# Performance work log

Hardware: AMD Instinct MI355X
Metric: run time of the kernel (lower is better)

Reference implementation:

```python
import jax, jax.numpy as jnp
import numpy as np

N = 8192
BOX = 50.0
CUTOFF = 5.0
MAX_E = 64 * N  # padded edge capacity (~34 avg neighbors expected)


def setup_inputs() -> dict:
    key = jax.random.key(0)
    pos = jax.random.uniform(key, (N, 3), dtype=jnp.float32) * BOX
    return {"pos": pos}


def _pairwise_dist(pos):
    # Euclidean cdist via the gram-matrix identity; avoids the [N,N,3] intermediate.
    sq = jnp.sum(pos * pos, axis=-1)                      # [N]
    d2 = sq[:, None] + sq[None, :] - 2.0 * (pos @ pos.T)  # [N,N]
    return jnp.sqrt(jnp.maximum(d2, 0.0))


def reference(pos):
    n = pos.shape[0]
    dist = _pairwise_dist(pos)
    # mask self-edges by pushing the diagonal above the cutoff (as in the torch code)
    dist = dist + (CUTOFF + 1.0) * jnp.eye(n, dtype=dist.dtype)
    mask = dist < CUTOFF
    # data-dependent nonzero -> fixed-size padded output for jit compatibility;
    # padded entries are filled with -1.
    rows, cols = jnp.nonzero(mask, size=MAX_E, fill_value=-1)
    return jnp.stack([rows, cols], axis=0)  # [2, MAX_E], int32
```

## Files before the change

### kernel.cpp

```cpp
#include <hip/hip_runtime.h>
#include <stdint.h>

#define N 8192
#define MAX_E (64 * N)
#define NCOL1 9
#define NCELLS (NCOL1 * NCOL1 * NCOL1)
#define CAP 40
#define RCAP 128
#define SCALE (9.0f / 50.0f)
#define POISON 0xAAAAAAAAu
#define M_WAVES 4
#define E_BLOCKS 256
#define E_ROWS 32

__device__ __forceinline__ float sq_exact(float x, float y, float z) {
    return __fadd_rn(__fadd_rn(__fmul_rn(x, x), __fmul_rn(y, y)), __fmul_rn(z, z));
}

__device__ __forceinline__ bool edge_pred(float xi, float yi, float zi, float sqi,
                                          float px, float py, float pz) {
    float sqj = sq_exact(px, py, pz);
    float dot = __fmaf_rn(zi, pz, __fmaf_rn(yi, py, __fmul_rn(xi, px)));
    float d2  = __fmaf_rn(-2.0f, dot, __fadd_rn(sqi, sqj));
    return d2 < 0x1.8ffffep+4f;
}

__device__ __forceinline__ int cell_of(float v) {
    int c = (int)(__fmul_rn(v, SCALE));
    return c > 8 ? 8 : c;
}

__device__ __forceinline__ int cell3_of(float x, float y, float z) {
    return (cell_of(x) * NCOL1 + cell_of(y)) * NCOL1 + cell_of(z);
}

__global__ __launch_bounds__(256) void bin_kernel(const float* __restrict__ posf,
                                                  unsigned* __restrict__ gcount,
                                                  float4* __restrict__ colpts) {
    const int i = blockIdx.x * 256 + threadIdx.x;
    float x = posf[3 * i], y = posf[3 * i + 1], z = posf[3 * i + 2];
    const int cell = cell3_of(x, y, z);
    unsigned p = atomicAdd(&gcount[cell], 1u) - POISON;
    if (p < CAP) {
        colpts[cell * CAP + p] = make_float4(x, y, z, __int_as_float(i));
    }
}

__global__ __launch_bounds__(256) void mask_kernel(const float* __restrict__ posf,
                                                   const unsigned* __restrict__ gcount,
                                                   const float4* __restrict__ colpts,
                                                   uint16_t* __restrict__ stage,
                                                   int* __restrict__ counts,
                                                   int* __restrict__ out) {
    __shared__ uint32_t lmask[M_WAVES][256];
    const int tid  = threadIdx.x;
    const int wave = tid >> 6;
    const int lane = tid & 63;
    const int row  = blockIdx.x * M_WAVES + wave;

    int2 neg; neg.x = -1; neg.y = -1;
    ((int2*)out)[blockIdx.x * 256 + tid] = neg;

#pragma unroll
    for (int k = lane; k < 256; k += 64) lmask[wave][k] = 0;
    __builtin_amdgcn_wave_barrier();

    const float xi = posf[3 * row], yi = posf[3 * row + 1], zi = posf[3 * row + 2];
    const float sqi = sq_exact(xi, yi, zi);
    const int cx = cell_of(xi), cy = cell_of(yi), cz = cell_of(zi);
    const int zlo = (cz > 0) ? cz - 1 : 0;
    const int zhi = (cz < 8) ? cz + 1 : 8;

    for (int dx = -1; dx <= 1; dx++) {
        const int nx = cx + dx;
        if ((unsigned)nx > 8u) continue;
        for (int dy = -1; dy <= 1; dy++) {
            const int ny = cy + dy;
            if ((unsigned)ny > 8u) continue;
            const int c0 = (nx * NCOL1 + ny) * NCOL1 + zlo;
            int l0 = (int)(gcount[c0] - POISON);     l0 = l0 > CAP ? CAP : l0;
            int l1 = (int)(gcount[c0 + 1] - POISON); l1 = l1 > CAP ? CAP : l1;
            int l2 = 0;
            if (zhi - zlo == 2) {
                l2 = (int)(gcount[c0 + 2] - POISON); l2 = l2 > CAP ? CAP : l2;
            }
            const int t01 = l0 + l1;
            const int tot = t01 + l2;
            for (int k = lane; k < tot; k += 64) {
                const int cellk = c0 + (k >= l0) + (k >= t01);
                const int off = k - ((k >= l0) ? l0 : 0) - ((k >= t01) ? l1 : 0);
                float4 pj = colpts[cellk * CAP + off];
                const int j = __float_as_int(pj.w);
                if (j != row && edge_pred(xi, yi, zi, sqi, pj.x, pj.y, pj.z))
                    atomicOr(&lmask[wave][j >> 5], 1u << (j & 31));
            }
        }
    }
    __builtin_amdgcn_wave_barrier();

    uint4 u = ((const uint4*)lmask[wave])[lane];
    uint64_t k0 = (uint64_t)u.x | ((uint64_t)u.y << 32);
    uint64_t k1 = (uint64_t)u.z | ((uint64_t)u.w << 32);
    const int pc = __popcll(k0) + __popcll(k1);
    int xs = pc;
#pragma unroll
    for (int o = 1; o < 64; o <<= 1) {
        int t = __shfl_up(xs, o);
        if (lane >= o) xs += t;
    }
    if (lane == 63) counts[row] = xs;
    int off = xs - pc;

    uint16_t* dst = stage + (size_t)row * RCAP;
    const int col0 = lane * 128;
    uint64_t m = k0;
    while (m) {
        int b = __ffsll((unsigned long long)m) - 1;
        m &= m - 1;
        if (off < RCAP) dst[off] = (uint16_t)(col0 + b);
        off++;
    }
    m = k1;
    while (m) {
        int b = __ffsll((unsigned long long)m) - 1;
        m &= m - 1;
        if (off < RCAP) dst[off] = (uint16_t)(col0 + 64 + b);
        off++;
    }
}

__global__ __launch_bounds__(256) void emit_kernel(const uint16_t* __restrict__ stage,
                                                   const int* __restrict__ counts,
                                                   int* __restrict__ out) {
    const int tid  = threadIdx.x;
    const int wave = tid >> 6;
    const int lane = tid & 63;
    const int row0 = blockIdx.x * E_ROWS;

    __shared__ int incl[256];
    __shared__ int wtot[4];
    __shared__ int excl32[32];

    const int4* c4 = (const int4*)counts;
    int s = 0;
#pragma unroll
    for (int k = 0; k < 8; k++) {
        int4 v = c4[tid * 8 + k];
        s += v.x + v.y + v.z + v.w;
    }
    int x = s;
#pragma unroll
    for (int o = 1; o < 64; o <<= 1) {
        int t = __shfl_up(x, o);
        if (lane >= o) x += t;
    }
    if (lane == 63) wtot[wave] = x;

    if (tid < 32) {
        int c = counts[row0 + tid];
        int y = c;
#pragma unroll
        for (int o = 1; o < 32; o <<= 1) {
            int t = __shfl_up(y, o, 32);
            if (tid >= o) y += t;
        }
        excl32[tid] = y - c;
    }
    __syncthreads();
    int woff = 0;
#pragma unroll
    for (int w = 0; w < 3; w++) woff += (wave > w) ? wtot[w] : 0;
    incl[tid] = woff + x;
    __syncthreads();
    const int base = (blockIdx.x > 0) ? incl[blockIdx.x - 1] : 0;

#pragma unroll
    for (int r = 0; r < 8; r++) {
        const int lr  = wave * 8 + r;
        const int row = row0 + lr;
        int c = counts[row];
        c = c > RCAP ? RCAP : c;
        const int slot = base + excl32[lr];
        const uint16_t* src = stage + (size_t)row * RCAP;
        for (int k = lane; k < c; k += 64) {
            const int sk = slot + k;
            if (sk < MAX_E) {
                out[sk] = row;
                out[MAX_E + sk] = (int)src[k];
            }
        }
    }
}

extern "C" void kernel_launch(void* const* d_in, const int* in_sizes, int n_in,
                              void* d_out, int out_size, void* d_ws, size_t ws_size,
                              hipStream_t stream) {
    const float* posf = (const float*)d_in[0];
    int* out = (int*)d_out;
    char* ws = (char*)d_ws;
    int*      counts = (int*)ws;
    unsigned* gcount = (unsigned*)(ws + (64 << 10));
    float4*   colpts = (float4*)(ws + (256 << 10));
    uint16_t* stage  = (uint16_t*)(ws + (1 << 20));

    bin_kernel<<<N / 256, 256, 0, stream>>>(posf, gcount, colpts);
    mask_kernel<<<N / M_WAVES, 256, 0, stream>>>(posf, gcount, colpts,
                                                 stage, counts, out);
    emit_kernel<<<E_BLOCKS, 256, 0, stream>>>(stage, counts, out);
}
```

Before: 74.52 us.

## Switch to compacted cell list with fine z-bins and contiguous neighbor ranges

Replaces the fixed-capacity 9x9x9 cell bins with a counting-sort cell list over 9x9x32 cells, using a count kernel, a prefix-scan and scatter kernel, and a global cell-base array. Each row in the mask kernel then scans one contiguous range per (x,y) column, covering only the z-cells within the cutoff margin. This cuts candidate pairs in z and removes the per-element cell and offset index math. The cost is an extra kernel launch and a redundant per-block prefix scan. It also relies on the workspace counters being poisoned to a known value.

```diff
diff --git a/kernel.cpp b/kernel.cpp
--- a/kernel.cpp
+++ b/kernel.cpp
@@ -4,10 +4,13 @@
 #define N 8192
 #define MAX_E (64 * N)
 #define NCOL1 9
-#define NCELLS (NCOL1 * NCOL1 * NCOL1)
-#define CAP 40
+#define NZ 32
+#define NCELLSF (NCOL1 * NCOL1 * NZ)
+#define CPT 11
 #define RCAP 128
 #define SCALE (9.0f / 50.0f)
+#define ZSCALE (32.0f / 50.0f)
+#define ZMARGIN 5.01f
 #define POISON 0xAAAAAAAAu
 #define M_WAVES 4
 #define E_BLOCKS 256
@@ -29,25 +32,74 @@
     int c = (int)(__fmul_rn(v, SCALE));
     return c > 8 ? 8 : c;
 }
-
-__device__ __forceinline__ int cell3_of(float x, float y, float z) {
-    return (cell_of(x) * NCOL1 + cell_of(y)) * NCOL1 + cell_of(z);
-}
-
-__global__ __launch_bounds__(256) void bin_kernel(const float* __restrict__ posf,
-                                                  unsigned* __restrict__ gcount,
-                                                  float4* __restrict__ colpts) {
+__device__ __forceinline__ int zcell_of(float v) {
+    int c = (int)(__fmul_rn(v, ZSCALE));
+    c = c < 0 ? 0 : c;
+    return c > (NZ - 1) ? (NZ - 1) : c;
+}
+__device__ __forceinline__ int cellf_of(float x, float y, float z) {
+    return (cell_of(x) * NCOL1 + cell_of(y)) * NZ + zcell_of(z);
+}
+
+__global__ __launch_bounds__(256) void count_kernel(const float* __restrict__ posf,
+                                                    unsigned* __restrict__ gcount) {
     const int i = blockIdx.x * 256 + threadIdx.x;
     float x = posf[3 * i], y = posf[3 * i + 1], z = posf[3 * i + 2];
-    const int cell = cell3_of(x, y, z);
-    unsigned p = atomicAdd(&gcount[cell], 1u) - POISON;
-    if (p < CAP) {
-        colpts[cell * CAP + p] = make_float4(x, y, z, __int_as_float(i));
-    }
+    atomicAdd(&gcount[cellf_of(x, y, z)], 1u);
+}
+
+__global__ __launch_bounds__(256) void scatter_kernel(const float* __restrict__ posf,
+                                                      const unsigned* __restrict__ gcount,
+                                                      unsigned* __restrict__ cursor,
+                                                      int* __restrict__ cbase_g,
+                                                      float4* __restrict__ colpts) {
+    __shared__ int cb[NCELLSF];
+    __shared__ int wtot[4];
+    const int tid  = threadIdx.x;
+    const int wave = tid >> 6;
+    const int lane = tid & 63;
+
+    int cnt[CPT];
+    int s = 0;
+#pragma unroll
+    for (int k = 0; k < CPT; k++) {
+        const int idx = tid * CPT + k;
+        cnt[k] = (idx < NCELLSF) ? (int)(gcount[idx] - POISON) : 0;
+        s += cnt[k];
+    }
+    int x = s;
+#pragma unroll
+    for (int o = 1; o < 64; o <<= 1) {
+        int t = __shfl_up(x, o);
+        if (lane >= o) x += t;
+    }
+    if (lane == 63) wtot[wave] = x;
+    __syncthreads();
+    int woff = 0;
+#pragma unroll
+    for (int w = 0; w < 3; w++) woff += (wave > w) ? wtot[w] : 0;
+    int run = woff + x - s;
+#pragma unroll
+    for (int k = 0; k < CPT; k++) {
+        const int idx = tid * CPT + k;
+        if (idx < NCELLSF) {
+            cb[idx] = run;
+            if (blockIdx.x == 0) cbase_g[idx] = run;
+            run += cnt[k];
+        }
+    }
+    if (blockIdx.x == 0 && tid == 255) cbase_g[NCELLSF] = woff + x;
+    __syncthreads();
+
+    const int i = blockIdx.x * 256 + tid;
+    float px = posf[3 * i], py = posf[3 * i + 1], pz = posf[3 * i + 2];
+    const int cell = cellf_of(px, py, pz);
+    const int slot = cb[cell] + (int)(atomicAdd(&cursor[cell], 1u) - POISON);
+    colpts[slot] = make_float4(px, py, pz, __int_as_float(i));
 }
 
 __global__ __launch_bounds__(256) void mask_kernel(const float* __restrict__ posf,
-                                                   const unsigned* __restrict__ gcount,
+                                                   const int* __restrict__ cbase,
                                                    const float4* __restrict__ colpts,
                                                    uint16_t* __restrict__ stage,
                                                    int* __restrict__ counts,
@@ -67,9 +119,9 @@
 
     const float xi = posf[3 * row], yi = posf[3 * row + 1], zi = posf[3 * row + 2];
     const float sqi = sq_exact(xi, yi, zi);
-    const int cx = cell_of(xi), cy = cell_of(yi), cz = cell_of(zi);
-    const int zlo = (cz > 0) ? cz - 1 : 0;
-    const int zhi = (cz < 8) ? cz + 1 : 8;
+    const int cx = cell_of(xi), cy = cell_of(yi);
+    const int zlo = zcell_of(__fadd_rn(zi, -ZMARGIN));
+    const int zhi = zcell_of(__fadd_rn(zi,  ZMARGIN));
 
     for (int dx = -1; dx <= 1; dx++) {
         const int nx = cx + dx;
@@ -77,19 +129,11 @@
         for (int dy = -1; dy <= 1; dy++) {
             const int ny = cy + dy;
             if ((unsigned)ny > 8u) continue;
-            const int c0 = (nx * NCOL1 + ny) * NCOL1 + zlo;
-            int l0 = (int)(gcount[c0] - POISON);     l0 = l0 > CAP ? CAP : l0;
-            int l1 = (int)(gcount[c0 + 1] - POISON); l1 = l1 > CAP ? CAP : l1;
-            int l2 = 0;
-            if (zhi - zlo == 2) {
-                l2 = (int)(gcount[c0 + 2] - POISON); l2 = l2 > CAP ? CAP : l2;
-            }
-            const int t01 = l0 + l1;
-            const int tot = t01 + l2;
-            for (int k = lane; k < tot; k += 64) {
-                const int cellk = c0 + (k >= l0) + (k >= t01);
-                const int off = k - ((k >= l0) ? l0 : 0) - ((k >= t01) ? l1 : 0);
-                float4 pj = colpts[cellk * CAP + off];
+            const int cw = (nx * NCOL1 + ny) * NZ;
+            const int s0 = cbase[cw + zlo];
+            const int e0 = cbase[cw + zhi + 1];
+            for (int k = s0 + lane; k < e0; k += 64) {
+                float4 pj = colpts[k];
                 const int j = __float_as_int(pj.w);
                 if (j != row && edge_pred(xi, yi, zi, sqi, pj.x, pj.y, pj.z))
                     atomicOr(&lmask[wave][j >> 5], 1u << (j & 31));
@@ -200,11 +244,14 @@
     char* ws = (char*)d_ws;
     int*      counts = (int*)ws;
     unsigned* gcount = (unsigned*)(ws + (64 << 10));
-    float4*   colpts = (float4*)(ws + (256 << 10));
+    unsigned* cursor = (unsigned*)(ws + (80 << 10));
+    int*      cbase  = (int*)(ws + (96 << 10));
+    float4*   colpts = (float4*)(ws + (128 << 10));
     uint16_t* stage  = (uint16_t*)(ws + (1 << 20));
 
-    bin_kernel<<<N / 256, 256, 0, stream>>>(posf, gcount, colpts);
-    mask_kernel<<<N / M_WAVES, 256, 0, stream>>>(posf, gcount, colpts,
+    count_kernel<<<N / 256, 256, 0, stream>>>(posf, gcount);
+    scatter_kernel<<<N / 256, 256, 0, stream>>>(posf, gcount, cursor, cbase, colpts);
+    mask_kernel<<<N / M_WAVES, 256, 0, stream>>>(posf, cbase, colpts,
                                                  stage, counts, out);
     emit_kernel<<<E_BLOCKS, 256, 0, stream>>>(stage, counts, out);
 }
```

Measured after the change: 75.58 us. Within noise of the previous version (+1.4%).
